# Kernel tuning notes

Measured on AMD Instinct MI355X. Metric: run time of the kernel, lower is better.

The kernel has to match this reference:

```python
import jax, jax.numpy as jnp
import numpy as np

EMBED_DIM = 1024
NUM_HEADS = 16
HEAD_DIM = EMBED_DIM // NUM_HEADS
BATCH = 2
SEQ = 2048


def setup_inputs() -> dict:
    key = jax.random.key(0)
    ks = jax.random.split(key, 9)
    scale = 1.0 / np.sqrt(EMBED_DIM)
    return {
        "inputs": jax.random.normal(ks[0], (BATCH, SEQ, EMBED_DIM), jnp.float32),
        "Wq": jax.random.normal(ks[1], (EMBED_DIM, EMBED_DIM), jnp.float32) * scale,
        "bq": jnp.zeros((EMBED_DIM,), jnp.float32),
        "Wk": jax.random.normal(ks[2], (EMBED_DIM, EMBED_DIM), jnp.float32) * scale,
        "bk": jnp.zeros((EMBED_DIM,), jnp.float32),
        "Wv": jax.random.normal(ks[3], (EMBED_DIM, EMBED_DIM), jnp.float32) * scale,
        "bv": jnp.zeros((EMBED_DIM,), jnp.float32),
        "Wo": jax.random.normal(ks[4], (EMBED_DIM, EMBED_DIM), jnp.float32) * scale,
        "bo": jnp.zeros((EMBED_DIM,), jnp.float32),
    }


def reference(inputs, Wq, bq, Wk, bk, Wv, bv, Wo, bo):
    B, S, D = inputs.shape
    H, Dh = NUM_HEADS, HEAD_DIM

    def split_heads(x):  # [B,S,D] -> [B,H,S,Dh]
        return x.reshape(B, S, H, Dh).transpose(0, 2, 1, 3)

    Q = split_heads(inputs @ Wq + bq)
    K = split_heads(inputs @ Wk + bk)
    V = split_heads(inputs @ Wv + bv)

    # naive full-score attention, faithful to the original
    scores = jnp.einsum("bhqd,bhkd->bhqk", Q, K) / jnp.sqrt(jnp.float32(Dh))
    weights = jax.nn.softmax(scores, axis=-1)
    out = jnp.einsum("bhqk,bhkd->bhqd", weights, V)

    concat = out.transpose(0, 2, 1, 3).reshape(B, S, D)
    return concat @ Wo + bo
```

## Files before the change

### kernel.cpp

```cpp
#include <hip/hip_runtime.h>

#define EMBED 1024
#define NHEAD 16
#define HDIM  64
#define BATCH 2
#define SEQ   2048
#define MTOK  (BATCH * SEQ)
#define QSCALE 0.1803368801f

typedef __bf16 bf16x8 __attribute__((ext_vector_type(8)));
typedef float  f32x4  __attribute__((ext_vector_type(4)));

__device__ __forceinline__ unsigned short f2bf(float f) {
  return (unsigned short)((__float_as_uint(f) + 0x8000u) >> 16);
}
__device__ __forceinline__ unsigned int pkbf(float a, float b) {
  unsigned int ua = __float_as_uint(a) + 0x8000u;
  unsigned int ub = __float_as_uint(b) + 0x8000u;
  return __builtin_amdgcn_perm(ub, ua, 0x07060302u);
}

__device__ __forceinline__ void gload_lds16(const unsigned short* g, unsigned short* l) {
  __builtin_amdgcn_global_load_lds((__attribute__((address_space(1))) void*)g,
                                   (__attribute__((address_space(3))) void*)l, 16, 0, 0);
}

__global__ __launch_bounds__(256)
void prep_k(const float* __restrict__ X, unsigned short* __restrict__ Xbf,
            const float* __restrict__ w0, const float* __restrict__ w1,
            const float* __restrict__ w2, const float* __restrict__ w3,
            unsigned short* __restrict__ t0, unsigned short* __restrict__ t1,
            unsigned short* __restrict__ t2, unsigned short* __restrict__ t3) {
  const int id = blockIdx.x;
  if (id < 4096) {
    int i = id * 256 + threadIdx.x;
    float4 f = reinterpret_cast<const float4*>(X)[i];
    reinterpret_cast<uint2*>(Xbf)[i] = make_uint2(pkbf(f.x, f.y), pkbf(f.z, f.w));
    return;
  }
  const int t = id - 4096;
  const float* s; unsigned short* d;
  switch (t >> 8) {
    case 0: s = w0; d = t0; break;
    case 1: s = w1; d = t1; break;
    case 2: s = w2; d = t2; break;
    default: s = w3; d = t3; break;
  }
  const int tt = t & 255;
  const int k0 = (tt >> 4) * 64, n0 = (tt & 15) * 64;
  __shared__ unsigned short T[64][65];
  for (int i = threadIdx.x; i < 4096; i += 256) {
    int r = i >> 6, c = i & 63;
    T[c][r] = f2bf(s[(size_t)(k0 + r) * EMBED + n0 + c]);
  }
  __syncthreads();
  for (int i = threadIdx.x; i < 4096; i += 256) {
    int r = i >> 6, c = i & 63;
    d[(size_t)(n0 + r) * EMBED + k0 + c] = T[r][c];
  }
}

template<int MODE, int BM>
__global__ void gemm_k(const unsigned short* __restrict__ A,
                       const unsigned short* __restrict__ Bt,
                       const float* __restrict__ b0, const float* __restrict__ b1,
                       const float* __restrict__ b2,
                       unsigned short* __restrict__ oQ, unsigned short* __restrict__ oK,
                       unsigned short* __restrict__ oV, float* __restrict__ oF) {
  constexpr int MI = BM / 32;
  __shared__ unsigned short As[BM][64];
  __shared__ unsigned short Bs[128][64];
  const int tid = threadIdx.x, lane = tid & 63, wave = tid >> 6;
  const int lr = lane & 15, quad = lane >> 4;
  const int wm = (wave >> 1) * (BM / 2), wn = (wave & 1) * 64;
  const int row0 = blockIdx.x * BM, col0 = blockIdx.y * 128;
  const int srow = lane >> 3, sc = lane & 7;
  const int sw0 = (quad ^ (lr & 7)) * 8;
  const int sw1 = ((quad ^ 4) ^ (lr & 7)) * 8;

  const f32x4 fz = {0.f, 0.f, 0.f, 0.f};
  f32x4 acc[MI][4];
#pragma unroll
  for (int i = 0; i < MI; ++i)
#pragma unroll
    for (int j = 0; j < 4; ++j) acc[i][j] = fz;

  for (int k0 = 0; k0 < EMBED; k0 += 64) {
#pragma unroll
    for (int g = 0; g < BM / 32; ++g) {
      int rbase = wave * (BM / 4) + g * 8;
      int row = rbase + srow;
      gload_lds16(&A[(size_t)(row0 + row) * EMBED + k0 + ((sc ^ (row & 7)) * 8)],
                  &As[rbase][0]);
    }
#pragma unroll
    for (int g = 0; g < 4; ++g) {
      int rbase = wave * 32 + g * 8;
      int row = rbase + srow;
      gload_lds16(&Bt[(size_t)(col0 + row) * EMBED + k0 + ((sc ^ (row & 7)) * 8)],
                  &Bs[rbase][0]);
    }
    __syncthreads();
#pragma unroll
    for (int kk = 0; kk < 64; kk += 32) {
      const int so = (kk == 0) ? sw0 : sw1;
      bf16x8 af[MI], bv[4];
#pragma unroll
      for (int i = 0; i < MI; ++i)
        af[i] = *reinterpret_cast<const bf16x8*>(&As[wm + i * 16 + lr][so]);
#pragma unroll
      for (int j = 0; j < 4; ++j)
        bv[j] = *reinterpret_cast<const bf16x8*>(&Bs[wn + j * 16 + lr][so]);
#pragma unroll
      for (int i = 0; i < MI; ++i)
#pragma unroll
        for (int j = 0; j < 4; ++j)
          acc[i][j] = __builtin_amdgcn_mfma_f32_16x16x32_bf16(af[i], bv[j],
                                                              acc[i][j], 0, 0, 0);
    }
    __syncthreads();
  }

#pragma unroll
  for (int i = 0; i < MI; ++i) {
#pragma unroll
    for (int j = 0; j < 4; ++j) {
      const int col = col0 + wn + j * 16 + lr;
      if (MODE == 1) {
        const float bb = b0[col];
#pragma unroll
        for (int r = 0; r < 4; ++r) {
          const int row = row0 + wm + i * 16 + quad * 4 + r;
          oF[((size_t)row << 10) + col] = acc[i][j][r] + bb;
        }
      } else {
        const int which = col >> 10, cn = col & 1023;
        const float bb = (which == 0 ? b0 : which == 1 ? b1 : b2)[cn];
        const float sscale = (which == 0) ? QSCALE : 1.0f;
        const int h = cn >> 6, dd = cn & 63;
#pragma unroll
        for (int r = 0; r < 4; ++r) {
          const int row = row0 + wm + i * 16 + quad * 4 + r;
          const int b = row >> 11, ss = row & (SEQ - 1);
          const float v = (acc[i][j][r] + bb) * sscale;
          if (which == 0) {
            oQ[((((size_t)b * NHEAD + h) * SEQ + ss) << 6) + dd] = f2bf(v);
          } else if (which == 1) {
            oK[((((size_t)b * NHEAD + h) * SEQ + ss) << 6) + dd] = f2bf(v);
          } else {
            oV[(((size_t)b * NHEAD + h) * HDIM + dd) * SEQ + ss] = f2bf(v);
          }
        }
      }
    }
  }
}

__global__ __launch_bounds__(256, 4)
void attn_k(const unsigned short* __restrict__ Qb,
            const unsigned short* __restrict__ Kb,
            const unsigned short* __restrict__ Vt,
            unsigned short* __restrict__ Ctx) {
  __shared__ unsigned short QPs[64][64];
  __shared__ unsigned short Ks[2][64][64];
  __shared__ unsigned short Vs[2][64][64];
  const int tid = threadIdx.x, lane = tid & 63, wave = tid >> 6;
  const int lr = lane & 15, quad = lane >> 4;
  const int bh = blockIdx.x, qt = blockIdx.y;
  const size_t base = (size_t)bh * SEQ * HDIM;
  const int srow = lane >> 3, sc = lane & 7;
  const int sw0 = (quad ^ (lr & 7)) * 8;
  const int sw1 = ((quad ^ 4) ^ (lr & 7)) * 8;

#pragma unroll
  for (int g = 0; g < 2; ++g) {
    int rbase = wave * 16 + g * 8;
    int row = rbase + srow;
    gload_lds16(&Qb[base + (size_t)(qt * 64 + row) * HDIM + ((sc ^ (row & 7)) * 8)],
                &QPs[rbase][0]);
    gload_lds16(&Kb[base + (size_t)row * HDIM + ((sc ^ (row & 7)) * 8)],
                &Ks[0][rbase][0]);
    gload_lds16(&Vt[base + (size_t)row * SEQ + ((sc ^ (row & 7)) * 8)],
                &Vs[0][rbase][0]);
  }
  __syncthreads();

  const bf16x8 qf0 = *reinterpret_cast<const bf16x8*>(&QPs[wave * 16 + lr][sw0]);
  const bf16x8 qf1 = *reinterpret_cast<const bf16x8*>(&QPs[wave * 16 + lr][sw1]);
  __threadfence_block();

  float l_part = 0.f;
  const f32x4 fz = {0.f, 0.f, 0.f, 0.f};
  f32x4 oacc[4] = {fz, fz, fz, fz};

  constexpr int NT = SEQ / 64;
  for (int kt = 0;;) {
    const int buf = kt & 1;

    if (kt + 1 < NT) {
#pragma unroll
      for (int g = 0; g < 2; ++g) {
        int rbase = wave * 16 + g * 8;
        int row = rbase + srow;
        gload_lds16(&Kb[base + (size_t)((kt + 1) * 64 + row) * HDIM + ((sc ^ (row & 7)) * 8)],
                    &Ks[buf ^ 1][rbase][0]);
        gload_lds16(&Vt[base + (size_t)row * SEQ + (kt + 1) * 64 + ((sc ^ (row & 7)) * 8)],
                    &Vs[buf ^ 1][rbase][0]);
      }
    }

    f32x4 sc4[4];
#pragma unroll
    for (int nt = 0; nt < 4; ++nt) {
      bf16x8 kf0 = *reinterpret_cast<const bf16x8*>(&Ks[buf][nt * 16 + lr][sw0]);
      bf16x8 kf1 = *reinterpret_cast<const bf16x8*>(&Ks[buf][nt * 16 + lr][sw1]);
      f32x4 a = __builtin_amdgcn_mfma_f32_16x16x32_bf16(kf0, qf0, fz, 0, 0, 0);
      sc4[nt] = __builtin_amdgcn_mfma_f32_16x16x32_bf16(kf1, qf1, a, 0, 0, 0);
    }

#pragma unroll
    for (int nt = 0; nt < 4; ++nt) {
      float p0 = __builtin_amdgcn_exp2f(sc4[nt][0]);
      float p1 = __builtin_amdgcn_exp2f(sc4[nt][1]);
      float p2 = __builtin_amdgcn_exp2f(sc4[nt][2]);
      float p3 = __builtin_amdgcn_exp2f(sc4[nt][3]);
      l_part += (p0 + p1) + (p2 + p3);
      const int pc = (nt * 2 + (quad >> 1)) ^ (lr & 7);
      *reinterpret_cast<uint2*>(&QPs[wave * 16 + lr][pc * 8 + (quad & 1) * 4]) =
          make_uint2(pkbf(p0, p1), pkbf(p2, p3));
    }

    __threadfence_block();

    const bf16x8 pa0 = *reinterpret_cast<const bf16x8*>(&QPs[wave * 16 + lr][sw0]);
    const bf16x8 pa1 = *reinterpret_cast<const bf16x8*>(&QPs[wave * 16 + lr][sw1]);
#pragma unroll
    for (int d = 0; d < 4; ++d) {
      bf16x8 vb0 = *reinterpret_cast<const bf16x8*>(&Vs[buf][d * 16 + lr][sw0]);
      bf16x8 vb1 = *reinterpret_cast<const bf16x8*>(&Vs[buf][d * 16 + lr][sw1]);
      oacc[d] = __builtin_amdgcn_mfma_f32_16x16x32_bf16(pa0, vb0, oacc[d], 0, 0, 0);
      oacc[d] = __builtin_amdgcn_mfma_f32_16x16x32_bf16(pa1, vb1, oacc[d], 0, 0, 0);
    }

    if (++kt == NT) break;
    __syncthreads();
  }

  l_part += __shfl_xor(l_part, 16);
  l_part += __shfl_xor(l_part, 32);

  const int b = bh >> 4, h = bh & 15;
  float linv[4];
#pragma unroll
  for (int r = 0; r < 4; ++r) linv[r] = 1.0f / __shfl(l_part, quad * 4 + r);
#pragma unroll
  for (int d = 0; d < 4; ++d)
#pragma unroll
    for (int r = 0; r < 4; ++r) {
      const int q = qt * 64 + wave * 16 + quad * 4 + r;
      Ctx[(((size_t)b * SEQ + q) << 10) + h * 64 + d * 16 + lr] =
          f2bf(oacc[d][r] * linv[r]);
    }
}

extern "C" void kernel_launch(void* const* d_in, const int* in_sizes, int n_in,
                              void* d_out, int out_size, void* d_ws, size_t ws_size,
                              hipStream_t stream) {
  const float* X  = (const float*)d_in[0];
  const float* Wq = (const float*)d_in[1];
  const float* bq = (const float*)d_in[2];
  const float* Wk = (const float*)d_in[3];
  const float* bk = (const float*)d_in[4];
  const float* Wv = (const float*)d_in[5];
  const float* bv = (const float*)d_in[6];
  const float* Wo = (const float*)d_in[7];
  const float* bo = (const float*)d_in[8];

  unsigned short* ws = (unsigned short*)d_ws;
  const size_t M1 = (size_t)1024 * 1024;
  unsigned short* Xbf = ws;
  unsigned short* WqT = ws + 4 * M1;
  unsigned short* WkT = ws + 5 * M1;
  unsigned short* WvT = ws + 6 * M1;
  unsigned short* WoT = ws + 7 * M1;
  unsigned short* Qb  = ws + 8 * M1;
  unsigned short* Kb  = ws + 12 * M1;
  unsigned short* Vt  = ws + 16 * M1;
  unsigned short* Ctx = ws + 20 * M1;

  prep_k<<<5120, 256, 0, stream>>>(X, Xbf, Wq, Wk, Wv, Wo, WqT, WkT, WvT, WoT);

  gemm_k<0, 128><<<dim3(MTOK / 128, 3072 / 128), 256, 0, stream>>>(
      Xbf, WqT, bq, bk, bv, Qb, Kb, Vt, nullptr);

  attn_k<<<dim3(BATCH * NHEAD, SEQ / 64), 256, 0, stream>>>(Qb, Kb, Vt, Ctx);

  gemm_k<1, 64><<<dim3(MTOK / 64, EMBED / 128), 256, 0, stream>>>(
      Ctx, WoT, bo, nullptr, nullptr, nullptr, nullptr, nullptr, (float*)d_out);
}
```

Baseline: 194.6 us.

## Double-buffer GEMM LDS tiles with larger 512-thread blocks and K=32 steps

Restructures the projection GEMMs to stage K=32 slices into double-buffered LDS so the next tile's global-to-LDS loads overlap the current MFMA work, with one barrier per step. Blocks grow to 512 threads (8 waves) with larger tiles (256x192 for QKV, 128x128 for the output projection), and wave priority is raised around the MFMA burst. This targets load latency and barrier stalls, but the QKV grid shrinks to 16x16 blocks, which may underfill the GPU, and the smaller K step doubles the number of loop iterations and barriers.

```diff
diff --git a/kernel.cpp b/kernel.cpp
--- a/kernel.cpp
+++ b/kernel.cpp
@@ -60,71 +60,89 @@
   }
 }
 
-template<int MODE, int BM>
-__global__ void gemm_k(const unsigned short* __restrict__ A,
-                       const unsigned short* __restrict__ Bt,
-                       const float* __restrict__ b0, const float* __restrict__ b1,
-                       const float* __restrict__ b2,
-                       unsigned short* __restrict__ oQ, unsigned short* __restrict__ oK,
-                       unsigned short* __restrict__ oV, float* __restrict__ oF) {
+template<int MODE, int BM, int BN>
+__global__ __launch_bounds__(512, 2)
+void gemm_k(const unsigned short* __restrict__ A,
+            const unsigned short* __restrict__ Bt,
+            const float* __restrict__ b0, const float* __restrict__ b1,
+            const float* __restrict__ b2,
+            unsigned short* __restrict__ oQ, unsigned short* __restrict__ oK,
+            unsigned short* __restrict__ oV, float* __restrict__ oF) {
   constexpr int MI = BM / 32;
-  __shared__ unsigned short As[BM][64];
-  __shared__ unsigned short Bs[128][64];
+  constexpr int NJ = BN / 64;
+  constexpr int AG = BM / 128;
+  constexpr int BG = (BN / 16 + 7) / 8;
+  constexpr int NT = EMBED / 32;
+
+  __shared__ unsigned short As[2][BM][32];
+  __shared__ unsigned short Bs[2][BN][32];
+
   const int tid = threadIdx.x, lane = tid & 63, wave = tid >> 6;
   const int lr = lane & 15, quad = lane >> 4;
-  const int wm = (wave >> 1) * (BM / 2), wn = (wave & 1) * 64;
-  const int row0 = blockIdx.x * BM, col0 = blockIdx.y * 128;
-  const int srow = lane >> 3, sc = lane & 7;
-  const int sw0 = (quad ^ (lr & 7)) * 8;
-  const int sw1 = ((quad ^ 4) ^ (lr & 7)) * 8;
+  const int wm = (wave >> 2) * (BM / 2);
+  const int wn = (wave & 3) * (BN / 4);
+  const int row0 = blockIdx.x * BM, col0 = blockIdx.y * BN;
+  const int srow = lane >> 2, sc = lane & 3;
+  const int scsw = (sc ^ ((srow >> 1) & 3)) * 8;
+  const int sw = (quad ^ ((lr >> 1) & 3)) * 8;
 
   const f32x4 fz = {0.f, 0.f, 0.f, 0.f};
-  f32x4 acc[MI][4];
+  f32x4 acc[MI][NJ];
 #pragma unroll
   for (int i = 0; i < MI; ++i)
 #pragma unroll
-    for (int j = 0; j < 4; ++j) acc[i][j] = fz;
-
-  for (int k0 = 0; k0 < EMBED; k0 += 64) {
-#pragma unroll
-    for (int g = 0; g < BM / 32; ++g) {
-      int rbase = wave * (BM / 4) + g * 8;
-      int row = rbase + srow;
-      gload_lds16(&A[(size_t)(row0 + row) * EMBED + k0 + ((sc ^ (row & 7)) * 8)],
-                  &As[rbase][0]);
-    }
-#pragma unroll
-    for (int g = 0; g < 4; ++g) {
-      int rbase = wave * 32 + g * 8;
-      int row = rbase + srow;
-      gload_lds16(&Bt[(size_t)(col0 + row) * EMBED + k0 + ((sc ^ (row & 7)) * 8)],
-                  &Bs[rbase][0]);
-    }
+    for (int j = 0; j < NJ; ++j) acc[i][j] = fz;
+
+  auto stage = [&](int bufi, int tt) {
+#pragma unroll
+    for (int g = 0; g < AG; ++g) {
+      int rbase = wave * (BM / 8) + g * 16;
+      gload_lds16(&A[(size_t)(row0 + rbase + srow) * EMBED + tt * 32 + scsw],
+                  &As[bufi][rbase][0]);
+    }
+#pragma unroll
+    for (int g = 0; g < BG; ++g) {
+      int slot = wave + 8 * g;
+      if (slot * 16 < BN) {
+        int rbase = slot * 16;
+        gload_lds16(&Bt[(size_t)(col0 + rbase + srow) * EMBED + tt * 32 + scsw],
+                    &Bs[bufi][rbase][0]);
+      }
+    }
+  };
+
+  stage(0, 0);
+  __syncthreads();
+
+  for (int t = 0;;) {
+    const int buf = t & 1;
+    if (t + 1 < NT) stage(buf ^ 1, t + 1);
+
+    bf16x8 af[MI], bv[NJ];
+#pragma unroll
+    for (int i = 0; i < MI; ++i)
+      af[i] = *reinterpret_cast<const bf16x8*>(&As[buf][wm + i * 16 + lr][sw]);
+#pragma unroll
+    for (int j = 0; j < NJ; ++j)
+      bv[j] = *reinterpret_cast<const bf16x8*>(&Bs[buf][wn + j * 16 + lr][sw]);
+
+    __builtin_amdgcn_s_setprio(1);
+#pragma unroll
+    for (int i = 0; i < MI; ++i)
+#pragma unroll
+      for (int j = 0; j < NJ; ++j)
+        acc[i][j] = __builtin_amdgcn_mfma_f32_16x16x32_bf16(af[i], bv[j],
+                                                            acc[i][j], 0, 0, 0);
+    __builtin_amdgcn_s_setprio(0);
+
+    if (++t == NT) break;
     __syncthreads();
-#pragma unroll
-    for (int kk = 0; kk < 64; kk += 32) {
-      const int so = (kk == 0) ? sw0 : sw1;
-      bf16x8 af[MI], bv[4];
-#pragma unroll
-      for (int i = 0; i < MI; ++i)
-        af[i] = *reinterpret_cast<const bf16x8*>(&As[wm + i * 16 + lr][so]);
-#pragma unroll
-      for (int j = 0; j < 4; ++j)
-        bv[j] = *reinterpret_cast<const bf16x8*>(&Bs[wn + j * 16 + lr][so]);
-#pragma unroll
-      for (int i = 0; i < MI; ++i)
-#pragma unroll
-        for (int j = 0; j < 4; ++j)
-          acc[i][j] = __builtin_amdgcn_mfma_f32_16x16x32_bf16(af[i], bv[j],
-                                                              acc[i][j], 0, 0, 0);
-    }
-    __syncthreads();
   }
 
 #pragma unroll
   for (int i = 0; i < MI; ++i) {
 #pragma unroll
-    for (int j = 0; j < 4; ++j) {
+    for (int j = 0; j < NJ; ++j) {
       const int col = col0 + wn + j * 16 + lr;
       if (MODE == 1) {
         const float bb = b0[col];
@@ -290,11 +308,11 @@
 
   prep_k<<<5120, 256, 0, stream>>>(X, Xbf, Wq, Wk, Wv, Wo, WqT, WkT, WvT, WoT);
 
-  gemm_k<0, 128><<<dim3(MTOK / 128, 3072 / 128), 256, 0, stream>>>(
+  gemm_k<0, 256, 192><<<dim3(MTOK / 256, 3072 / 192), 512, 0, stream>>>(
       Xbf, WqT, bq, bk, bv, Qb, Kb, Vt, nullptr);
 
   attn_k<<<dim3(BATCH * NHEAD, SEQ / 64), 256, 0, stream>>>(Qb, Kb, Vt, Ctx);
 
-  gemm_k<1, 64><<<dim3(MTOK / 64, EMBED / 128), 256, 0, stream>>>(
+  gemm_k<1, 128, 128><<<dim3(MTOK / 128, EMBED / 128), 512, 0, stream>>>(
       Ctx, WoT, bo, nullptr, nullptr, nullptr, nullptr, nullptr, (float*)d_out);
 }
```

New measurement: 219.9 us. 1.13x slower.
